# Kernel tuning notes

Measured on AMD Instinct MI355X. Metric: run time of the kernel, lower is better.

Reference implementation:

```python
import jax, jax.numpy as jnp
import numpy as np

M_IND = 1024   # inducing points
K_NN = 16      # nearest neighbors
JITTER = 1e-4


def rbf(X, Z):
    # unit-variance, unit-lengthscale RBF kernel; returns (K, squared distances)
    sq = jnp.sum(X * X, -1)[:, None] + jnp.sum(Z * Z, -1)[None, :] - 2.0 * (X @ Z.T)
    sq = jnp.maximum(sq, 0.0)
    return jnp.exp(-0.5 * sq), sq


def setup_inputs() -> dict:
    key = jax.random.key(0)
    k1, k2, k3 = jax.random.split(key, 3)
    return {
        "X": jax.random.normal(k1, (65536, 3), jnp.float32),
        "Z": jax.random.normal(k2, (M_IND, 3), jnp.float32),
        "Lu_raw": jax.random.normal(k3, (M_IND, M_IND), jnp.float32),
        "mu": jnp.zeros((M_IND,), jnp.float32),
    }


def reference(X, Z, Lu_raw, mu):
    N = X.shape[0]
    Kxx = jnp.ones((N,), X.dtype)                      # diag of RBF(X,X) is 1
    Kxz, dist = rbf(X, Z)                              # [N,M], [N,M]
    Kzz, _ = rbf(Z, Z)                                 # [M,M]

    # transform_to(lower_cholesky): strict lower triangle + exp(diag)
    Lu = jnp.tril(Lu_raw, -1) + jnp.diag(jnp.exp(jnp.diag(Lu_raw)))

    eyeM = jnp.eye(M_IND, dtype=X.dtype)
    L = jnp.linalg.cholesky(Kzz + JITTER * eyeM)       # [M,M]
    Kzz_j = L @ L.T                                    # == little_L @ little_L.T math (Kzz + jitter*I)
    Su = Lu @ Lu.T                                     # full variational covariance

    # K nearest inducing points per data point (argsort(dist)[:, :K])
    _, idx = jax.lax.top_k(-dist, K_NN)                # [N,K]

    lKzz = Kzz_j[idx[:, :, None], idx[:, None, :]]     # [N,K,K] gathered submatrices
    lS = Su[idx[:, :, None], idx[:, None, :]]          # [N,K,K]
    lKxz = jnp.take_along_axis(Kxz, idx, axis=1)       # [N,K]
    lmu = mu[idx]                                      # [N,K]

    eyeK = jnp.eye(K_NN, dtype=X.dtype)
    inv = jnp.linalg.inv(lKzz + JITTER * eyeK)         # batched tiny inverses [N,K,K]
    W = jnp.einsum('nk,nkj->nj', lKxz, inv)            # [N,K]

    mean = jnp.einsum('nk,nk->n', W, lmu)              # [N]
    cov = (Kxx
           - jnp.einsum('ni,nij,nj->n', W, lKzz, W)
           + jnp.einsum('ni,nij,nj->n', W, lS, W))
    std = jnp.sqrt(jnp.clip(cov, 0.05, None))          # qF scale = clamp(cov, 0.05)**0.5
    return jnp.stack([mean, std])                      # [2,N] qF parameters
```

## Files before the change

### kernel.cpp

```cpp
#include <hip/hip_runtime.h>
#include <math.h>

#define N_PTS 65536
#define M_IND 1024
#define KNN 16
#define JITTER 1e-4f

#define PACKED_FLOATS (M_IND * (M_IND + 1) / 2)
#define PACKED_BYTES  ((size_t)PACKED_FLOATS * sizeof(float))

#define TSU 32
#define SU_BLOCKS 528
#define PTS_PER_BLK 128
#define QSTRIDE 17
#define GRID_BLKS (N_PTS / PTS_PER_BLK)


__device__ __forceinline__ void su_tile(const float* __restrict__ Lu_raw,
                                        float* __restrict__ P,
                                        int bid, int tid,
                                        float (*As)[36], float (*Bs)[36]) {
    int rt = (int)((sqrtf(8.0f * (float)bid + 1.0f) - 1.0f) * 0.5f);
    while ((rt + 1) * (rt + 2) / 2 <= bid) ++rt;
    while (rt * (rt + 1) / 2 > bid) --rt;
    int ct = bid - rt * (rt + 1) / 2;
    int i0 = rt * TSU, j0 = ct * TSU;

    int tx = tid & 15, ty = tid >> 4;
    int sr = tid >> 3, sc = (tid & 7) << 2;
    float a00 = 0.f, a01 = 0.f, a10 = 0.f, a11 = 0.f;

    int nch = ct + 1;
    int gi = i0 + sr, gj = j0 + sr;
    float4 pa = *(const float4*)(Lu_raw + (unsigned)gi * M_IND + sc);
    float4 pb = *(const float4*)(Lu_raw + (unsigned)gj * M_IND + sc);

    for (int c = 0; c < nch; ++c) {
        int gk = (c << 5) + sc;
        float aa[4] = {pa.x, pa.y, pa.z, pa.w};
        float bb[4] = {pb.x, pb.y, pb.z, pb.w};
        #pragma unroll
        for (int q = 0; q < 4; ++q) {
            int k = gk + q;
            aa[q] = (k < gi) ? aa[q] : ((k == gi) ? __expf(aa[q]) : 0.0f);
            bb[q] = (k < gj) ? bb[q] : ((k == gj) ? __expf(bb[q]) : 0.0f);
        }
        *(float4*)&As[sr][sc] = make_float4(aa[0], aa[1], aa[2], aa[3]);
        *(float4*)&Bs[sr][sc] = make_float4(bb[0], bb[1], bb[2], bb[3]);
        __syncthreads();
        if (c + 1 < nch) {
            int kn = ((c + 1) << 5) + sc;
            pa = *(const float4*)(Lu_raw + (unsigned)gi * M_IND + kn);
            pb = *(const float4*)(Lu_raw + (unsigned)gj * M_IND + kn);
        }
        #pragma unroll
        for (int kk = 0; kk < 32; kk += 4) {
            float4 av0 = *(const float4*)&As[ty][kk];
            float4 av1 = *(const float4*)&As[ty + 16][kk];
            float4 bv0 = *(const float4*)&Bs[tx][kk];
            float4 bv1 = *(const float4*)&Bs[tx + 16][kk];
            a00 = fmaf(av0.x, bv0.x, fmaf(av0.y, bv0.y, fmaf(av0.z, bv0.z, fmaf(av0.w, bv0.w, a00))));
            a01 = fmaf(av0.x, bv1.x, fmaf(av0.y, bv1.y, fmaf(av0.z, bv1.z, fmaf(av0.w, bv1.w, a01))));
            a10 = fmaf(av1.x, bv0.x, fmaf(av1.y, bv0.y, fmaf(av1.z, bv0.z, fmaf(av1.w, bv0.w, a10))));
            a11 = fmaf(av1.x, bv1.x, fmaf(av1.y, bv1.y, fmaf(av1.z, bv1.z, fmaf(av1.w, bv1.w, a11))));
        }
        __syncthreads();
    }

    int ia = i0 + ty, ib = i0 + ty + 16;
    int ja = j0 + tx, jb = j0 + tx + 16;
    if (ja <= ia) P[((unsigned)ia * (ia + 1) >> 1) + ja] = a00;
    if (jb <= ia) P[((unsigned)ia * (ia + 1) >> 1) + jb] = a01;
    if (ja <= ib) P[((unsigned)ib * (ib + 1) >> 1) + ja] = a10;
    if (jb <= ib) P[((unsigned)ib * (ib + 1) >> 1) + jb] = a11;
}

__global__ __launch_bounds__(256) void su_kernel(const float* __restrict__ Lu_raw,
                                                 float* __restrict__ P) {
    __shared__ float As[TSU][36];
    __shared__ float Bs[TSU][36];
    su_tile(Lu_raw, P, blockIdx.x, threadIdx.x, As, Bs);
}

__device__ __forceinline__ void ce(unsigned long long& x, unsigned long long& y) {
    unsigned long long a = x, b = y;
    bool c = a < b;
    x = c ? a : b;
    y = c ? b : a;
}
__device__ __forceinline__ void ce(float& x, float& y) {
    float a = fminf(x, y), b = fmaxf(x, y);
    x = a; y = b;
}

template <typename KT>
__device__ __forceinline__ void sort16(KT* a) {
    #pragma unroll
    for (int p = 1; p < 16; p <<= 1)
        #pragma unroll
        for (int k = p; k >= 1; k >>= 1)
            #pragma unroll
            for (int j = k & (p - 1); j + k < 16; j += 2 * k)
                #pragma unroll
                for (int i = 0; i < k; ++i)
                    if (i + j + k < 16)
                        if (((i + j) / (2 * p)) == ((i + j + k) / (2 * p)))
                            ce(a[i + j], a[i + j + k]);
}

template <typename KT>
__device__ __forceinline__ void cleanup16(KT* a) {
    #pragma unroll
    for (int d = 8; d >= 1; d >>= 1)
        #pragma unroll
        for (int i = 0; i < 16; ++i)
            if ((i & d) == 0) ce(a[i], a[i | d]);
}

__device__ __forceinline__ float uval(float4 z, float xn0, float xn1, float xn2) {
    return fmaf(xn0, z.x, fmaf(xn1, z.y, fmaf(xn2, z.z, z.w)));
}

template <int MODE>
__global__ __launch_bounds__(256, 2) void vnngp_kernel(const float* __restrict__ X,
                                                       const float* __restrict__ Z,
                                                       const float* __restrict__ mu,
                                                       float* __restrict__ P,
                                                       const float* __restrict__ Lu_raw,
                                                       unsigned int* __restrict__ ctr,
                                                       float* __restrict__ out) {
    __shared__ __align__(16) char smem[37888];
    float4* Zs = (float4*)smem;
    float* mus = (float*)(smem + 16384);
    unsigned long long* qb = (unsigned long long*)(smem + 20480);
    int tid = threadIdx.x;

    for (int r = tid; r < M_IND; r += 256) {
        float zx = Z[r * 3 + 0], zy = Z[r * 3 + 1], zz = Z[r * 3 + 2];
        Zs[r] = make_float4(zx, zy, zz, 0.5f * (zx * zx + zy * zy + zz * zz));
        mus[r] = mu[r];
    }

    if (MODE == 2) {
        float (*As)[36] = (float (*)[36])(smem + 20480);
        float (*Bs)[36] = (float (*)[36])(smem + 20480 + 4608);
        int t = blockIdx.x;
        #pragma unroll
        for (int r = 16; r < 32; ++r) {
            int s = (r * (r + 1)) >> 1;
            if (t >= s) ++t;
        }
        su_tile(Lu_raw, P, t, tid, As, Bs);
        if (blockIdx.x < 16) {
            int r = 16 + blockIdx.x;
            su_tile(Lu_raw, P, (r * (r + 1)) >> 1, tid, As, Bs);
        }
        __syncthreads();
        if (tid == 0) {
            __threadfence();
            atomicAdd(ctr, 1u);
        }
    } else {
        __syncthreads();
    }

    {
        int pt = tid >> 2, sub = tid & 3;
        int nA = blockIdx.x * PTS_PER_BLK + pt;
        int nB = nA + 64;
        float xA0 = X[nA * 3 + 0], xA1 = X[nA * 3 + 1], xA2 = X[nA * 3 + 2];
        float xB0 = X[nB * 3 + 0], xB1 = X[nB * 3 + 1], xB2 = X[nB * 3 + 2];
        float xqA = fmaf(xA0, xA0, fmaf(xA1, xA1, xA2 * xA2));
        float xqB = fmaf(xB0, xB0, fmaf(xB1, xB1, xB2 * xB2));
        float nA0 = -xA0, nA1 = -xA1, nA2 = -xA2;
        float nB0 = -xB0, nB1 = -xB1, nB2 = -xB2;
        int mbase = sub << 8;
        int rot = sub << 1;

        float TA[16], TB[16];
        #pragma unroll
        for (int j = 0; j < 16; ++j) { TA[j] = 3.4e38f; TB[j] = 3.4e38f; }
        #pragma unroll 1
        for (int c = 0; c < 16; ++c) {
            int base = mbase + (c << 4);
            #pragma unroll
            for (int j = 0; j < 16; ++j) {
                int m = base + ((j + rot) & 15);
                float4 z = Zs[m];
                TA[j] = fminf(TA[j], uval(z, nA0, nA1, nA2));
                TB[j] = fminf(TB[j], uval(z, nB0, nB1, nB2));
            }
        }
        sort16(TA);
        sort16(TB);
        #pragma unroll
        for (int round = 1; round <= 2; round <<= 1) {
            float oA[16], oB[16];
            #pragma unroll
            for (int i = 0; i < 16; ++i) {
                oA[i] = __shfl_xor(TA[i], round, 64);
                oB[i] = __shfl_xor(TB[i], round, 64);
            }
            #pragma unroll
            for (int i = 0; i < 16; ++i) {
                TA[i] = fminf(TA[i], oA[15 - i]);
                TB[i] = fminf(TB[i], oB[15 - i]);
            }
            cleanup16(TA);
            cleanup16(TB);
        }
        float TstarA = TA[15], TstarB = TB[15];

        unsigned short* mycA = ((unsigned short*)qb) + pt * (QSTRIDE * 4) + sub * 16;
        unsigned short* mycB = ((unsigned short*)qb) + (pt + 64) * (QSTRIDE * 4) + sub * 16;
        int cntA = 0, cntB = 0;
        #pragma unroll 1
        for (int c = 0; c < 16; ++c) {
            int base = mbase + (c << 4);
            #pragma unroll
            for (int j = 0; j < 16; ++j) {
                int m = base + ((j + rot) & 15);
                float4 z = Zs[m];
                float uA = uval(z, nA0, nA1, nA2);
                float uB = uval(z, nB0, nB1, nB2);
                if (uA <= TstarA) { if (cntA < 16) mycA[cntA] = (unsigned short)m; ++cntA; }
                if (uB <= TstarB) { if (cntB < 16) mycB[cntB] = (unsigned short)m; ++cntB; }
            }
        }

        int ovfA = cntA > 16 ? 1 : 0;
        ovfA |= __shfl_xor(ovfA, 1, 64);
        ovfA |= __shfl_xor(ovfA, 2, 64);
        int ovfB = cntB > 16 ? 1 : 0;
        ovfB |= __shfl_xor(ovfB, 1, 64);
        ovfB |= __shfl_xor(ovfB, 2, 64);

        if (!ovfA) {
            const unsigned long long* m64 = (const unsigned long long*)mycA;
            unsigned long long raw[4] = {m64[0], m64[1], m64[2], m64[3]};
            unsigned long long C[16];
            #pragma unroll
            for (int i = 0; i < 16; ++i) {
                int m = (int)((raw[i >> 2] >> ((i & 3) * 16)) & 0x3FF);
                float u = uval(Zs[m], nA0, nA1, nA2);
                float d = fmaxf(fmaf(2.0f, u, xqA), 0.0f);
                unsigned long long key =
                    ((unsigned long long)__float_as_uint(d) << 32) | (unsigned)m;
                C[i] = (i < cntA) ? key : ~0ULL;
            }
            sort16(C);
            #pragma unroll
            for (int round = 1; round <= 2; round <<= 1) {
                unsigned long long o[16];
                #pragma unroll
                for (int i = 0; i < 16; ++i) o[i] = __shfl_xor(C[i], round, 64);
                #pragma unroll
                for (int i = 0; i < 16; ++i) {
                    unsigned long long b = o[15 - i];
                    C[i] = C[i] < b ? C[i] : b;
                }
                cleanup16(C);
            }
            if (sub == 0) {
                #pragma unroll
                for (int i = 0; i < 16; ++i) qb[pt * QSTRIDE + i] = C[i];
            }
        } else if (sub == 0) {
            unsigned long long R[16];
            #pragma unroll
            for (int i = 0; i < 16; ++i) R[i] = ~0ULL;
            for (int m = 0; m < M_IND; ++m) {
                float u = uval(Zs[m], nA0, nA1, nA2);
                float d = fmaxf(fmaf(2.0f, u, xqA), 0.0f);
                unsigned long long kk =
                    ((unsigned long long)__float_as_uint(d) << 32) | (unsigned)m;
                if (kk < R[15]) {
                    #pragma unroll
                    for (int j = 0; j < 16; ++j) {
                        unsigned long long t = R[j];
                        bool cc = kk < t;
                        R[j] = cc ? kk : t;
                        kk = cc ? t : kk;
                    }
                }
            }
            #pragma unroll
            for (int i = 0; i < 16; ++i) qb[pt * QSTRIDE + i] = R[i];
        }

        if (!ovfB) {
            const unsigned long long* m64 = (const unsigned long long*)mycB;
            unsigned long long raw[4] = {m64[0], m64[1], m64[2], m64[3]};
            unsigned long long C[16];
            #pragma unroll
            for (int i = 0; i < 16; ++i) {
                int m = (int)((raw[i >> 2] >> ((i & 3) * 16)) & 0x3FF);
                float u = uval(Zs[m], nB0, nB1, nB2);
                float d = fmaxf(fmaf(2.0f, u, xqB), 0.0f);
                unsigned long long key =
                    ((unsigned long long)__float_as_uint(d) << 32) | (unsigned)m;
                C[i] = (i < cntB) ? key : ~0ULL;
            }
            sort16(C);
            #pragma unroll
            for (int round = 1; round <= 2; round <<= 1) {
                unsigned long long o[16];
                #pragma unroll
                for (int i = 0; i < 16; ++i) o[i] = __shfl_xor(C[i], round, 64);
                #pragma unroll
                for (int i = 0; i < 16; ++i) {
                    unsigned long long b = o[15 - i];
                    C[i] = C[i] < b ? C[i] : b;
                }
                cleanup16(C);
            }
            if (sub == 0) {
                #pragma unroll
                for (int i = 0; i < 16; ++i) qb[(pt + 64) * QSTRIDE + i] = C[i];
            }
        } else if (sub == 0) {
            unsigned long long R[16];
            #pragma unroll
            for (int i = 0; i < 16; ++i) R[i] = ~0ULL;
            for (int m = 0; m < M_IND; ++m) {
                float u = uval(Zs[m], nB0, nB1, nB2);
                float d = fmaxf(fmaf(2.0f, u, xqB), 0.0f);
                unsigned long long kk =
                    ((unsigned long long)__float_as_uint(d) << 32) | (unsigned)m;
                if (kk < R[15]) {
                    #pragma unroll
                    for (int j = 0; j < 16; ++j) {
                        unsigned long long t = R[j];
                        bool cc = kk < t;
                        R[j] = cc ? kk : t;
                        kk = cc ? t : kk;
                    }
                }
            }
            #pragma unroll
            for (int i = 0; i < 16; ++i) qb[(pt + 64) * QSTRIDE + i] = R[i];
        }
    }
    __syncthreads();

    if (MODE == 2) {
        if (tid == 0) {
            while (__hip_atomic_load(ctr, __ATOMIC_ACQUIRE, __HIP_MEMORY_SCOPE_AGENT)
                   < (unsigned)GRID_BLKS)
                __builtin_amdgcn_s_sleep(8);
        }
        __syncthreads();
    }
    if (tid >= PTS_PER_BLK) return;

    int n = blockIdx.x * PTS_PER_BLK + tid;
    int idx[KNN];
    float kv[KNN];
    float nx[KNN], ny[KNN], nz[KNN], nq[KNN];
    #pragma unroll
    for (int a = 0; a < KNN; ++a) {
        unsigned long long k = qb[tid * QSTRIDE + a];
        idx[a] = (int)(k & 0xFFFFFFFFULL);
        float d = __uint_as_float((unsigned)(k >> 32));
        kv[a] = __expf(-0.5f * d);
        float4 z = Zs[idx[a]];
        nx[a] = z.x; ny[a] = z.y; nz[a] = z.z; nq[a] = z.w;
    }

    float A[KNN * (KNN + 1) / 2];
    #pragma unroll
    for (int r = 0; r < KNN; ++r) {
        A[r * (r + 1) / 2 + r] = 1.0f + 2.0f * JITTER;
        #pragma unroll
        for (int c = 0; c < r; ++c) {
            float dot = fmaf(nx[r], nx[c], fmaf(ny[r], ny[c], nz[r] * nz[c]));
            A[r * (r + 1) / 2 + c] = __expf(fminf(dot - nq[r] - nq[c], 0.0f));
        }
    }

    #pragma unroll
    for (int c = 0; c < KNN; ++c) {
        float diag = A[c * (c + 1) / 2 + c];
        #pragma unroll
        for (int k = 0; k < c; ++k) {
            float l = A[c * (c + 1) / 2 + k];
            diag = fmaf(-l, l, diag);
        }
        float rinv = __frsqrt_rn(fmaxf(diag, 1e-12f));
        A[c * (c + 1) / 2 + c] = rinv;
        #pragma unroll
        for (int r = c + 1; r < KNN; ++r) {
            float v = A[r * (r + 1) / 2 + c];
            #pragma unroll
            for (int k = 0; k < c; ++k)
                v = fmaf(-A[r * (r + 1) / 2 + k], A[c * (c + 1) / 2 + k], v);
            A[r * (r + 1) / 2 + c] = v * rinv;
        }
    }

    float w[KNN];
    #pragma unroll
    for (int r = 0; r < KNN; ++r) {
        float v = kv[r];
        #pragma unroll
        for (int c = 0; c < r; ++c) v = fmaf(-A[r * (r + 1) / 2 + c], w[c], v);
        w[r] = v * A[r * (r + 1) / 2 + r];
    }
    #pragma unroll
    for (int r = KNN - 1; r >= 0; --r) {
        float v = w[r];
        #pragma unroll
        for (int c = r + 1; c < KNN; ++c) v = fmaf(-A[c * (c + 1) / 2 + r], w[c], v);
        w[r] = v * A[r * (r + 1) / 2 + r];
    }

    float wk = 0.f, ww = 0.f, mean = 0.f;
    #pragma unroll
    for (int a = 0; a < KNN; ++a) {
        wk = fmaf(w[a], kv[a], wk);
        ww = fmaf(w[a], w[a], ww);
        mean = fmaf(w[a], mus[idx[a]], mean);
    }

    float qs = 0.f;
    if (MODE != 0) {
        #pragma unroll
        for (int r = 0; r < KNN; ++r) {
            int a = idx[r];
            float wr = w[r];
            float rowacc = 0.f;
            #pragma unroll
            for (int c = 0; c < r; ++c) {
                int b = idx[c];
                int hi = a > b ? a : b;
                int lo = a > b ? b : a;
                rowacc = fmaf(w[c], P[((unsigned)hi * (hi + 1) >> 1) + lo], rowacc);
            }
            qs = fmaf(wr, fmaf(wr, P[((unsigned)a * (a + 1) >> 1) + a], 2.0f * rowacc), qs);
        }
    } else {
        int si[KNN]; float sw[KNN];
        #pragma unroll
        for (int a = 0; a < KNN; ++a) { si[a] = idx[a]; sw[a] = w[a]; }
        #pragma unroll
        for (int a = 1; a < KNN; ++a) {
            int iv = si[a]; float wv = sw[a];
            int b = a - 1;
            while (b >= 0 && si[b] > iv) { si[b + 1] = si[b]; sw[b + 1] = sw[b]; --b; }
            si[b + 1] = iv; sw[b + 1] = wv;
        }
        int s = 0;
        int kend = si[KNN - 1];
        for (int k = 0; k <= kend; ++k) {
            float v = 0.f;
            if (s < KNN && si[s] == k) {
                v = sw[s] * __expf(Lu_raw[(unsigned)k * M_IND + k]);
                ++s;
            }
            for (int a = s; a < KNN; ++a)
                v = fmaf(sw[a], Lu_raw[(unsigned)si[a] * M_IND + k], v);
            qs = fmaf(v, v, qs);
        }
    }

    float cov = 1.0f - (wk - JITTER * ww) + qs;
    float sd = sqrtf(fmaxf(cov, 0.05f));
    out[n] = mean;
    out[N_PTS + n] = sd;
}

extern "C" void kernel_launch(void* const* d_in, const int* in_sizes, int n_in,
                              void* d_out, int out_size, void* d_ws, size_t ws_size,
                              hipStream_t stream) {
    const float* X      = (const float*)d_in[0];
    const float* Z      = (const float*)d_in[1];
    const float* Lu_raw = (const float*)d_in[2];
    const float* mu     = (const float*)d_in[3];
    float* out = (float*)d_out;

    if (ws_size >= PACKED_BYTES + 64) {
        float* P = (float*)d_ws;
        unsigned int* ctr = (unsigned int*)((char*)d_ws + PACKED_BYTES);
        hipMemsetAsync(ctr, 0, sizeof(unsigned int), stream);
        vnngp_kernel<2><<<GRID_BLKS, 256, 0, stream>>>(X, Z, mu, P, Lu_raw, ctr, out);
    } else if (ws_size >= PACKED_BYTES) {
        float* P = (float*)d_ws;
        su_kernel<<<SU_BLOCKS, 256, 0, stream>>>(Lu_raw, P);
        vnngp_kernel<1><<<GRID_BLKS, 256, 0, stream>>>(X, Z, mu, P, Lu_raw, nullptr, out);
    } else {
        vnngp_kernel<0><<<GRID_BLKS, 256, 0, stream>>>(X, Z, mu, nullptr, Lu_raw, nullptr, out);
    }
}
```

Baseline: 163.0 us.

## Split long Su tiles across blocks with atomic accumulation and add spin-wait timeout

Su tiles with long K-loops (column tile index 16 or higher) are now split in two. The block that owns the tile computes the first 16 chunks, and 136 extra block assignments compute the remaining chunks and add their partial results with float atomics. This is meant to balance per-block Su work before the grid-wide barrier. The cost is a memset of the whole packed buffer before every launch, plus the atomic traffic. A bounded spin with a fallback that skips the Su term is also added, which could silently drop part of the covariance if the timeout triggers.

```diff
diff --git a/kernel.cpp b/kernel.cpp
--- a/kernel.cpp
+++ b/kernel.cpp
@@ -14,28 +14,24 @@
 #define PTS_PER_BLK 128
 #define QSTRIDE 17
 #define GRID_BLKS (N_PTS / PTS_PER_BLK)
-
-
-__device__ __forceinline__ void su_tile(const float* __restrict__ Lu_raw,
-                                        float* __restrict__ P,
-                                        int bid, int tid,
-                                        float (*As)[36], float (*Bs)[36]) {
-    int rt = (int)((sqrtf(8.0f * (float)bid + 1.0f) - 1.0f) * 0.5f);
-    while ((rt + 1) * (rt + 2) / 2 <= bid) ++rt;
-    while (rt * (rt + 1) / 2 > bid) --rt;
-    int ct = bid - rt * (rt + 1) / 2;
+#define SPIN_MAX 32768
+
+
+__device__ __forceinline__ void su_range(const float* __restrict__ Lu_raw,
+                                         float* __restrict__ P,
+                                         int rt, int ct, int c0, int c1,
+                                         bool atomic, int tid,
+                                         float (*As)[36], float (*Bs)[36]) {
     int i0 = rt * TSU, j0 = ct * TSU;
-
     int tx = tid & 15, ty = tid >> 4;
     int sr = tid >> 3, sc = (tid & 7) << 2;
     float a00 = 0.f, a01 = 0.f, a10 = 0.f, a11 = 0.f;
 
-    int nch = ct + 1;
     int gi = i0 + sr, gj = j0 + sr;
-    float4 pa = *(const float4*)(Lu_raw + (unsigned)gi * M_IND + sc);
-    float4 pb = *(const float4*)(Lu_raw + (unsigned)gj * M_IND + sc);
-
-    for (int c = 0; c < nch; ++c) {
+    float4 pa = *(const float4*)(Lu_raw + (unsigned)gi * M_IND + (c0 << 5) + sc);
+    float4 pb = *(const float4*)(Lu_raw + (unsigned)gj * M_IND + (c0 << 5) + sc);
+
+    for (int c = c0; c < c1; ++c) {
         int gk = (c << 5) + sc;
         float aa[4] = {pa.x, pa.y, pa.z, pa.w};
         float bb[4] = {pb.x, pb.y, pb.z, pb.w};
@@ -48,7 +44,7 @@
         *(float4*)&As[sr][sc] = make_float4(aa[0], aa[1], aa[2], aa[3]);
         *(float4*)&Bs[sr][sc] = make_float4(bb[0], bb[1], bb[2], bb[3]);
         __syncthreads();
-        if (c + 1 < nch) {
+        if (c + 1 < c1) {
             int kn = ((c + 1) << 5) + sc;
             pa = *(const float4*)(Lu_raw + (unsigned)gi * M_IND + kn);
             pb = *(const float4*)(Lu_raw + (unsigned)gj * M_IND + kn);
@@ -69,10 +65,28 @@
 
     int ia = i0 + ty, ib = i0 + ty + 16;
     int ja = j0 + tx, jb = j0 + tx + 16;
-    if (ja <= ia) P[((unsigned)ia * (ia + 1) >> 1) + ja] = a00;
-    if (jb <= ia) P[((unsigned)ia * (ia + 1) >> 1) + jb] = a01;
-    if (ja <= ib) P[((unsigned)ib * (ib + 1) >> 1) + ja] = a10;
-    if (jb <= ib) P[((unsigned)ib * (ib + 1) >> 1) + jb] = a11;
+    if (atomic) {
+        if (ja <= ia) atomicAdd(&P[((unsigned)ia * (ia + 1) >> 1) + ja], a00);
+        if (jb <= ia) atomicAdd(&P[((unsigned)ia * (ia + 1) >> 1) + jb], a01);
+        if (ja <= ib) atomicAdd(&P[((unsigned)ib * (ib + 1) >> 1) + ja], a10);
+        if (jb <= ib) atomicAdd(&P[((unsigned)ib * (ib + 1) >> 1) + jb], a11);
+    } else {
+        if (ja <= ia) P[((unsigned)ia * (ia + 1) >> 1) + ja] = a00;
+        if (jb <= ia) P[((unsigned)ia * (ia + 1) >> 1) + jb] = a01;
+        if (ja <= ib) P[((unsigned)ib * (ib + 1) >> 1) + ja] = a10;
+        if (jb <= ib) P[((unsigned)ib * (ib + 1) >> 1) + jb] = a11;
+    }
+}
+
+__device__ __forceinline__ void su_tile(const float* __restrict__ Lu_raw,
+                                        float* __restrict__ P,
+                                        int bid, int tid,
+                                        float (*As)[36], float (*Bs)[36]) {
+    int rt = (int)((sqrtf(8.0f * (float)bid + 1.0f) - 1.0f) * 0.5f);
+    while ((rt + 1) * (rt + 2) / 2 <= bid) ++rt;
+    while (rt * (rt + 1) / 2 > bid) --rt;
+    int ct = bid - rt * (rt + 1) / 2;
+    su_range(Lu_raw, P, rt, ct, 0, ct + 1, false, tid, As, Bs);
 }
 
 __global__ __launch_bounds__(256) void su_kernel(const float* __restrict__ Lu_raw,
@@ -129,10 +143,11 @@
                                                        const float* __restrict__ Lu_raw,
                                                        unsigned int* __restrict__ ctr,
                                                        float* __restrict__ out) {
-    __shared__ __align__(16) char smem[37888];
+    __shared__ __align__(16) char smem[37904];
     float4* Zs = (float4*)smem;
     float* mus = (float*)(smem + 16384);
     unsigned long long* qb = (unsigned long long*)(smem + 20480);
+    int* flagp = (int*)(smem + 37888);
     int tid = threadIdx.x;
 
     for (int r = tid; r < M_IND; r += 256) {
@@ -150,10 +165,22 @@
             int s = (r * (r + 1)) >> 1;
             if (t >= s) ++t;
         }
-        su_tile(Lu_raw, P, t, tid, As, Bs);
+        int rt = (int)((sqrtf(8.0f * (float)t + 1.0f) - 1.0f) * 0.5f);
+        while ((rt + 1) * (rt + 2) / 2 <= t) ++rt;
+        while (rt * (rt + 1) / 2 > t) --rt;
+        int ct = t - rt * (rt + 1) / 2;
+        bool sp = (ct >= 16);
+        su_range(Lu_raw, P, rt, ct, 0, sp ? 16 : (ct + 1), sp, tid, As, Bs);
         if (blockIdx.x < 16) {
             int r = 16 + blockIdx.x;
-            su_tile(Lu_raw, P, (r * (r + 1)) >> 1, tid, As, Bs);
+            su_range(Lu_raw, P, r, 0, 0, 1, false, tid, As, Bs);
+        }
+        if (blockIdx.x < 136) {
+            int h = 135 - blockIdx.x;
+            int rt2 = 16, cum = 0;
+            while (h >= cum + (rt2 - 15)) { cum += (rt2 - 15); ++rt2; }
+            int ct2 = 16 + (h - cum);
+            su_range(Lu_raw, P, rt2, ct2, 16, ct2 + 1, true, tid, As, Bs);
         }
         __syncthreads();
         if (tid == 0) {
@@ -277,10 +304,10 @@
                 if (kk < R[15]) {
                     #pragma unroll
                     for (int j = 0; j < 16; ++j) {
-                        unsigned long long t = R[j];
-                        bool cc = kk < t;
-                        R[j] = cc ? kk : t;
-                        kk = cc ? t : kk;
+                        unsigned long long t2 = R[j];
+                        bool cc = kk < t2;
+                        R[j] = cc ? kk : t2;
+                        kk = cc ? t2 : kk;
                     }
                 }
             }
@@ -330,10 +357,10 @@
                 if (kk < R[15]) {
                     #pragma unroll
                     for (int j = 0; j < 16; ++j) {
-                        unsigned long long t = R[j];
-                        bool cc = kk < t;
-                        R[j] = cc ? kk : t;
-                        kk = cc ? t : kk;
+                        unsigned long long t2 = R[j];
+                        bool cc = kk < t2;
+                        R[j] = cc ? kk : t2;
+                        kk = cc ? t2 : kk;
                     }
                 }
             }
@@ -343,13 +370,19 @@
     }
     __syncthreads();
 
+    bool havP = (MODE == 1);
     if (MODE == 2) {
         if (tid == 0) {
+            int ok = 1, iters = 0;
             while (__hip_atomic_load(ctr, __ATOMIC_ACQUIRE, __HIP_MEMORY_SCOPE_AGENT)
-                   < (unsigned)GRID_BLKS)
+                   < (unsigned)GRID_BLKS) {
                 __builtin_amdgcn_s_sleep(8);
+                if (++iters > SPIN_MAX) { ok = 0; break; }
+            }
+            *flagp = ok;
         }
         __syncthreads();
+        havP = (*flagp != 0);
     }
     if (tid >= PTS_PER_BLK) return;
 
@@ -383,8 +416,8 @@
         float diag = A[c * (c + 1) / 2 + c];
         #pragma unroll
         for (int k = 0; k < c; ++k) {
-            float l = A[c * (c + 1) / 2 + k];
-            diag = fmaf(-l, l, diag);
+            float lv = A[c * (c + 1) / 2 + k];
+            diag = fmaf(-lv, lv, diag);
         }
         float rinv = __frsqrt_rn(fmaxf(diag, 1e-12f));
         A[c * (c + 1) / 2 + c] = rinv;
@@ -423,7 +456,7 @@
     }
 
     float qs = 0.f;
-    if (MODE != 0) {
+    if (MODE != 0 && havP) {
         #pragma unroll
         for (int r = 0; r < KNN; ++r) {
             int a = idx[r];
@@ -481,6 +514,7 @@
     if (ws_size >= PACKED_BYTES + 64) {
         float* P = (float*)d_ws;
         unsigned int* ctr = (unsigned int*)((char*)d_ws + PACKED_BYTES);
+        hipMemsetAsync(P, 0, PACKED_BYTES, stream);
         hipMemsetAsync(ctr, 0, sizeof(unsigned int), stream);
         vnngp_kernel<2><<<GRID_BLKS, 256, 0, stream>>>(X, Z, mu, P, Lu_raw, ctr, out);
     } else if (ws_size >= PACKED_BYTES) {
```

Measured after the change: 164.8 us. About the same (+1.1%).
